# Performance work log

Hardware: AMD Instinct MI355X
Metric: run time of the kernel (lower is better)

Reference implementation:

```python
import jax, jax.numpy as jnp
import numpy as np

NUM_EDGES = 800_000
NUM_VERTICES = 100_000
NNZ = 1_600_000
D_MODEL = 128


def setup_inputs() -> dict:
    key = jax.random.key(0)
    ks = jax.random.split(key, 10)
    d = D_MODEL
    return {
        "x_e": jax.random.normal(ks[0], (NUM_EDGES, d), dtype=jnp.float32),
        "h_v": jax.random.normal(ks[1], (NUM_VERTICES, d), dtype=jnp.float32),
        "c_v": jax.random.normal(ks[2], (NUM_VERTICES, d), dtype=jnp.float32),
        "W_ih": jax.random.normal(ks[3], (4 * d, d), dtype=jnp.float32) * 0.05,
        "W_hh": jax.random.normal(ks[4], (4 * d, d), dtype=jnp.float32) * 0.05,
        "b_ih": jax.random.normal(ks[5], (4 * d,), dtype=jnp.float32) * 0.05,
        "b_hh": jax.random.normal(ks[6], (4 * d,), dtype=jnp.float32) * 0.05,
        "nnz_edge_ids": jax.random.randint(ks[7], (NNZ,), 0, NUM_EDGES, dtype=jnp.int32),
        "nnz_vertex_ids": jax.random.randint(ks[8], (NNZ,), 0, NUM_VERTICES, dtype=jnp.int32),
        "v_batch": jax.random.randint(ks[9], (NUM_VERTICES,), 0, 8, dtype=jnp.int32),
    }


def reference(x_e, h_v, c_v, W_ih, W_hh, b_ih, b_hh, nnz_edge_ids, nnz_vertex_ids, v_batch):
    # msg = adj_t.T @ x_e : scatter-add edge embeddings into incident vertices
    msg = jax.ops.segment_sum(x_e[nnz_edge_ids], nnz_vertex_ids,
                              num_segments=h_v.shape[0])  # [V, d]
    # single-step LSTM update (PyTorch gate order: i, f, g, o)
    gates = msg @ W_ih.T + b_ih + h_v @ W_hh.T + b_hh  # [V, 4d]
    i, f, g, o = jnp.split(gates, 4, axis=-1)
    i = jax.nn.sigmoid(i)
    f = jax.nn.sigmoid(f)
    g = jnp.tanh(g)
    o = jax.nn.sigmoid(o)
    c_new = f * c_v + i * g
    h_new = o * jnp.tanh(c_new)
    return (h_new, c_new)
```

## Files before the change

### kernel.cpp

```cpp
#include <hip/hip_runtime.h>
#include <hip/hip_bf16.h>

#define NE 800000
#define NV 100000
#define NNZN 1600000
#define D 128
#define SLOT_CAP 64

typedef short short8 __attribute__((ext_vector_type(8)));
typedef short s16x4 __attribute__((ext_vector_type(4)));
typedef float f32x4 __attribute__((ext_vector_type(4)));
typedef int   i32x4 __attribute__((ext_vector_type(4)));

__device__ __forceinline__ unsigned short f2bfu(float f) {
  union { float f; unsigned u; } x;
  x.f = f;
  unsigned u = x.u;
  u += ((u >> 16) & 1u) + 0x7FFFu;
  return (unsigned short)(u >> 16);
}

__device__ __forceinline__ float fsigmoid(float x) {
  return 1.0f / (1.0f + __expf(-x));
}
__device__ __forceinline__ float ftanh(float x) {
  return 2.0f / (1.0f + __expf(-2.0f * x)) - 1.0f;
}

__global__ __launch_bounds__(256) void wconv_kernel(
    const float* __restrict__ W_ih, const float* __restrict__ W_hh,
    const float* __restrict__ b_ih, const float* __restrict__ b_hh,
    short* __restrict__ Wcat, float* __restrict__ bcomb,
    int* __restrict__ counts) {
  int idx = blockIdx.x * 256 + threadIdx.x;
  if (idx < 16384) {
    int c8 = idx;
    int pos = c8 & 63;
    int t   = (c8 >> 6) & 1;
    int g   = (c8 >> 7) & 3;
    int kk  = (c8 >> 9) & 7;
    int wid = (c8 >> 12) & 3;
    int n = g * 128 + wid * 32 + t * 16 + (pos >> 2);
    int k0 = kk * 32 + (pos & 3) * 8;
    const float* src = (k0 < 128) ? (W_ih + (size_t)n * 128 + k0)
                                  : (W_hh + (size_t)n * 128 + (k0 - 128));
    f32x4 a = *(const f32x4*)(src);
    f32x4 b = *(const f32x4*)(src + 4);
    short8 v;
    v[0] = (short)f2bfu(a[0]); v[1] = (short)f2bfu(a[1]);
    v[2] = (short)f2bfu(a[2]); v[3] = (short)f2bfu(a[3]);
    v[4] = (short)f2bfu(b[0]); v[5] = (short)f2bfu(b[1]);
    v[6] = (short)f2bfu(b[2]); v[7] = (short)f2bfu(b[3]);
    *(short8*)(Wcat + (size_t)c8 * 8) = v;
  }
  if (idx < 512) bcomb[idx] = b_ih[idx] + b_hh[idx];
  if (idx < NV) counts[idx] = 0;
}

__global__ __launch_bounds__(256) void scatter_direct_kernel(
    const int* __restrict__ eid, const int* __restrict__ vid,
    int* __restrict__ counts, int* __restrict__ slots) {
  int j = blockIdx.x * 256 + threadIdx.x;
  if (j < NNZN) {
    int v = vid[j];
    int pos = atomicAdd(&counts[v], 1);
    if (pos < SLOT_CAP) slots[(size_t)v * SLOT_CAP + pos] = eid[j];
  }
}

__global__ __launch_bounds__(256, 6) void gather_kernel(
    const float* __restrict__ x_e, const int* __restrict__ counts,
    const int* __restrict__ slots, char* __restrict__ msgb) {
  __shared__ int slds[4][SLOT_CAP];
  const int tid = threadIdx.x;
  const int wid = tid >> 6;
  const int lane = tid & 63;
  const int v = blockIdx.x * 4 + wid;
  const int half = lane >> 5;
  const int pos = lane & 31;
  int deg = counts[v];
  deg = deg > SLOT_CAP ? SLOT_CAP : deg;
  slds[wid][lane] = slots[(size_t)v * SLOT_CAP + lane];
  const int* row_ids = slds[wid];

  f32x4 a0 = {0.f, 0.f, 0.f, 0.f}, a1 = a0, a2 = a0, a3 = a0;
  const int nfull = deg >> 4;
  const int rem = deg & 15;
#pragma unroll 1
  for (int c = 0; c < nfull; ++c) {
    int b = c * 16 + half;
    int e0 = row_ids[b];      int e1 = row_ids[b + 2];
    int e2 = row_ids[b + 4];  int e3 = row_ids[b + 6];
    int e4 = row_ids[b + 8];  int e5 = row_ids[b + 10];
    int e6 = row_ids[b + 12]; int e7 = row_ids[b + 14];
    f32x4 t0 = *(const f32x4*)(x_e + (size_t)e0 * D + pos * 4);
    f32x4 t1 = *(const f32x4*)(x_e + (size_t)e1 * D + pos * 4);
    f32x4 t2 = *(const f32x4*)(x_e + (size_t)e2 * D + pos * 4);
    f32x4 t3 = *(const f32x4*)(x_e + (size_t)e3 * D + pos * 4);
    f32x4 t4 = *(const f32x4*)(x_e + (size_t)e4 * D + pos * 4);
    f32x4 t5 = *(const f32x4*)(x_e + (size_t)e5 * D + pos * 4);
    f32x4 t6 = *(const f32x4*)(x_e + (size_t)e6 * D + pos * 4);
    f32x4 t7 = *(const f32x4*)(x_e + (size_t)e7 * D + pos * 4);
    a0 += t0; a1 += t1; a2 += t2; a3 += t3;
    a0 += t4; a1 += t5; a2 += t6; a3 += t7;
  }
  if (rem) {
    int b = nfull * 16 + half;
    f32x4 z = {0.f, 0.f, 0.f, 0.f};
    int i0 = b,      i1 = b + 2,  i2 = b + 4,  i3 = b + 6;
    int i4 = b + 8,  i5 = b + 10, i6 = b + 12, i7 = b + 14;
    int e0 = row_ids[i0 < deg ? i0 : 0];
    int e1 = row_ids[i1 < deg ? i1 : 0];
    int e2 = row_ids[i2 < deg ? i2 : 0];
    int e3 = row_ids[i3 < deg ? i3 : 0];
    int e4 = row_ids[i4 < deg ? i4 : 0];
    int e5 = row_ids[i5 < deg ? i5 : 0];
    int e6 = row_ids[i6 < deg ? i6 : 0];
    int e7 = row_ids[i7 < deg ? i7 : 0];
    f32x4 t0 = *(const f32x4*)(x_e + (size_t)e0 * D + pos * 4);
    f32x4 t1 = *(const f32x4*)(x_e + (size_t)e1 * D + pos * 4);
    f32x4 t2 = *(const f32x4*)(x_e + (size_t)e2 * D + pos * 4);
    f32x4 t3 = *(const f32x4*)(x_e + (size_t)e3 * D + pos * 4);
    f32x4 t4 = *(const f32x4*)(x_e + (size_t)e4 * D + pos * 4);
    f32x4 t5 = *(const f32x4*)(x_e + (size_t)e5 * D + pos * 4);
    f32x4 t6 = *(const f32x4*)(x_e + (size_t)e6 * D + pos * 4);
    f32x4 t7 = *(const f32x4*)(x_e + (size_t)e7 * D + pos * 4);
    a0 += (i0 < deg) ? t0 : z;
    a1 += (i1 < deg) ? t1 : z;
    a2 += (i2 < deg) ? t2 : z;
    a3 += (i3 < deg) ? t3 : z;
    a0 += (i4 < deg) ? t4 : z;
    a1 += (i5 < deg) ? t5 : z;
    a2 += (i6 < deg) ? t6 : z;
    a3 += (i7 < deg) ? t7 : z;
  }
  a0 += a1;
  a2 += a3;
  a0 += a2;
  f32x4 b;
  b[0] = __shfl_xor(a0[0], 32);
  b[1] = __shfl_xor(a0[1], 32);
  b[2] = __shfl_xor(a0[2], 32);
  b[3] = __shfl_xor(a0[3], 32);
  a0 += b;
  if (half == 0) {
    s16x4 p;
    p[0] = (short)f2bfu(a0[0]);
    p[1] = (short)f2bfu(a0[1]);
    p[2] = (short)f2bfu(a0[2]);
    p[3] = (short)f2bfu(a0[3]);
    *(s16x4*)(msgb + (size_t)v * 512 + pos * 8) = p;
  }
}

__global__ __launch_bounds__(256) void lstm_kernel(
    const char* __restrict__ msgb, const float* __restrict__ h_v,
    const float* __restrict__ c_v, const short* __restrict__ Wcat,
    const float* __restrict__ bcomb, float* __restrict__ out) {
  __shared__ char Atile[32 * 256 * 2];
  const int tid = threadIdx.x;
  const int vbase = blockIdx.x * 32;

#pragma unroll
  for (int i = 0; i < 4; ++i) {
    int cid = tid + i * 256;
    int row = cid >> 5;
    int c = cid & 31;
    short8 v;
    if (c < 16) {
      v = *(const short8*)(msgb + (size_t)(vbase + row) * 512 + c * 16);
    } else {
      const float* src = h_v + (size_t)(vbase + row) * D + (c - 16) * 8;
      f32x4 a = *(const f32x4*)(src);
      f32x4 b = *(const f32x4*)(src + 4);
      v[0] = (short)f2bfu(a[0]); v[1] = (short)f2bfu(a[1]);
      v[2] = (short)f2bfu(a[2]); v[3] = (short)f2bfu(a[3]);
      v[4] = (short)f2bfu(b[0]); v[5] = (short)f2bfu(b[1]);
      v[6] = (short)f2bfu(b[2]); v[7] = (short)f2bfu(b[3]);
    }
    int byteoff = (row * 512 + c * 16) ^ ((row & 7) << 4);
    *(short8*)(Atile + byteoff) = v;
  }
  __syncthreads();

  const int wid = tid >> 6;
  const int lane = tid & 63;
  const int l16 = lane & 15;
  const int lhi = lane >> 4;

  f32x4 acc[2][4][2] = {};

#pragma unroll
  for (int kk = 0; kk < 8; ++kk) {
    short8 afrag[2];
#pragma unroll
    for (int m = 0; m < 2; ++m) {
      int row = m * 16 + l16;
      int byteoff = (row * 512 + kk * 64 + lhi * 16) ^ ((row & 7) << 4);
      afrag[m] = *(const short8*)(Atile + byteoff);
    }
#pragma unroll
    for (int g = 0; g < 4; ++g) {
#pragma unroll
      for (int t = 0; t < 2; ++t) {
        size_t boff = (size_t)(wid * 64 + kk * 8 + g * 2 + t) * 1024
                    + (size_t)(l16 * 4 + lhi) * 16;
        short8 bfrag = *(const short8*)((const char*)Wcat + boff);
        acc[0][g][t] = __builtin_amdgcn_mfma_f32_16x16x32_bf16(afrag[0], bfrag, acc[0][g][t], 0, 0, 0);
        acc[1][g][t] = __builtin_amdgcn_mfma_f32_16x16x32_bf16(afrag[1], bfrag, acc[1][g][t], 0, 0, 0);
      }
    }
  }

  float* out_h = out;
  float* out_c = out + (size_t)NV * D;
#pragma unroll
  for (int m = 0; m < 2; ++m) {
#pragma unroll
    for (int t = 0; t < 2; ++t) {
      int d = wid * 32 + t * 16 + l16;
      float bi = bcomb[d];
      float bf = bcomb[128 + d];
      float bg = bcomb[256 + d];
      float bo = bcomb[384 + d];
#pragma unroll
      for (int r = 0; r < 4; ++r) {
        int v = vbase + m * 16 + lhi * 4 + r;
        float gi = acc[m][0][t][r] + bi;
        float gf = acc[m][1][t][r] + bf;
        float gg = acc[m][2][t][r] + bg;
        float go = acc[m][3][t][r] + bo;
        float ii = fsigmoid(gi);
        float ff = fsigmoid(gf);
        float g_ = ftanh(gg);
        float oo = fsigmoid(go);
        float cv = c_v[(size_t)v * D + d];
        float cn = ff * cv + ii * g_;
        float hn = oo * ftanh(cn);
        out_h[(size_t)v * D + d] = hn;
        out_c[(size_t)v * D + d] = cn;
      }
    }
  }
}

extern "C" void kernel_launch(void* const* d_in, const int* in_sizes, int n_in,
                              void* d_out, int out_size, void* d_ws, size_t ws_size,
                              hipStream_t stream) {
  const float* x_e  = (const float*)d_in[0];
  const float* h_v  = (const float*)d_in[1];
  const float* c_v  = (const float*)d_in[2];
  const float* W_ih = (const float*)d_in[3];
  const float* W_hh = (const float*)d_in[4];
  const float* b_ih = (const float*)d_in[5];
  const float* b_hh = (const float*)d_in[6];
  const int* eid    = (const int*)d_in[7];
  const int* vid    = (const int*)d_in[8];
  float* out = (float*)d_out;

  char* w = (char*)d_ws;
  short* Wcat  = (short*)w;                 w += 512 * 256 * sizeof(short);
  float* bcomb = (float*)w;                 w += 512 * sizeof(float);
  int* counts  = (int*)w;                   w += NV * sizeof(int);
  int* slots   = (int*)w;

  char* msgb = (char*)(out + (size_t)NV * D);

  wconv_kernel<<<512, 256, 0, stream>>>(W_ih, W_hh, b_ih, b_hh, Wcat, bcomb, counts);
  scatter_direct_kernel<<<(NNZN + 255) / 256, 256, 0, stream>>>(eid, vid, counts, slots);
  gather_kernel<<<NV / 4, 256, 0, stream>>>(x_e, counts, slots, msgb);
  lstm_kernel<<<NV / 32, 256, 0, stream>>>(msgb, h_v, c_v, Wcat, bcomb, out);
}
```

Before: 418.6 us.

## Split gather into two edge-range passes for cache locality

The gather runs as two passes, each touching only half of the x_e edge rows, so each pass works on about 205 MB of x_e instead of 410 MB and is meant to get better last-level cache hit rates. The first pass writes fp32 partial sums into the output buffer, and the second pass adds its half, converts to bf16 and writes msgb. The cost is reading counts and slots twice, extra partial-sum traffic, and wasted loads of a placeholder row for edges outside the range. Half the x_e set is still larger than MI355X's documented 256 MB Infinity Cache, so the locality gain may be small.

```diff
diff --git a/kernel.cpp b/kernel.cpp
--- a/kernel.cpp
+++ b/kernel.cpp
@@ -68,9 +68,11 @@
   }
 }
 
-__global__ __launch_bounds__(256, 6) void gather_kernel(
+template <bool FIRST>
+__global__ __launch_bounds__(256, 6) void gather_pass_kernel(
     const float* __restrict__ x_e, const int* __restrict__ counts,
-    const int* __restrict__ slots, char* __restrict__ msgb) {
+    const int* __restrict__ slots, float* __restrict__ pf,
+    char* __restrict__ msgb, int lo, int hi) {
   __shared__ int slds[4][SLOT_CAP];
   const int tid = threadIdx.x;
   const int wid = tid >> 6;
@@ -82,31 +84,14 @@
   deg = deg > SLOT_CAP ? SLOT_CAP : deg;
   slds[wid][lane] = slots[(size_t)v * SLOT_CAP + lane];
   const int* row_ids = slds[wid];
+  const float* clamp_row = x_e + (size_t)lo * D + pos * 4;
 
   f32x4 a0 = {0.f, 0.f, 0.f, 0.f}, a1 = a0, a2 = a0, a3 = a0;
-  const int nfull = deg >> 4;
-  const int rem = deg & 15;
+  const f32x4 z = a0;
+  const int nvol = (deg + 15) >> 4;
 #pragma unroll 1
-  for (int c = 0; c < nfull; ++c) {
+  for (int c = 0; c < nvol; ++c) {
     int b = c * 16 + half;
-    int e0 = row_ids[b];      int e1 = row_ids[b + 2];
-    int e2 = row_ids[b + 4];  int e3 = row_ids[b + 6];
-    int e4 = row_ids[b + 8];  int e5 = row_ids[b + 10];
-    int e6 = row_ids[b + 12]; int e7 = row_ids[b + 14];
-    f32x4 t0 = *(const f32x4*)(x_e + (size_t)e0 * D + pos * 4);
-    f32x4 t1 = *(const f32x4*)(x_e + (size_t)e1 * D + pos * 4);
-    f32x4 t2 = *(const f32x4*)(x_e + (size_t)e2 * D + pos * 4);
-    f32x4 t3 = *(const f32x4*)(x_e + (size_t)e3 * D + pos * 4);
-    f32x4 t4 = *(const f32x4*)(x_e + (size_t)e4 * D + pos * 4);
-    f32x4 t5 = *(const f32x4*)(x_e + (size_t)e5 * D + pos * 4);
-    f32x4 t6 = *(const f32x4*)(x_e + (size_t)e6 * D + pos * 4);
-    f32x4 t7 = *(const f32x4*)(x_e + (size_t)e7 * D + pos * 4);
-    a0 += t0; a1 += t1; a2 += t2; a3 += t3;
-    a0 += t4; a1 += t5; a2 += t6; a3 += t7;
-  }
-  if (rem) {
-    int b = nfull * 16 + half;
-    f32x4 z = {0.f, 0.f, 0.f, 0.f};
     int i0 = b,      i1 = b + 2,  i2 = b + 4,  i3 = b + 6;
     int i4 = b + 8,  i5 = b + 10, i6 = b + 12, i7 = b + 14;
     int e0 = row_ids[i0 < deg ? i0 : 0];
@@ -117,22 +102,30 @@
     int e5 = row_ids[i5 < deg ? i5 : 0];
     int e6 = row_ids[i6 < deg ? i6 : 0];
     int e7 = row_ids[i7 < deg ? i7 : 0];
-    f32x4 t0 = *(const f32x4*)(x_e + (size_t)e0 * D + pos * 4);
-    f32x4 t1 = *(const f32x4*)(x_e + (size_t)e1 * D + pos * 4);
-    f32x4 t2 = *(const f32x4*)(x_e + (size_t)e2 * D + pos * 4);
-    f32x4 t3 = *(const f32x4*)(x_e + (size_t)e3 * D + pos * 4);
-    f32x4 t4 = *(const f32x4*)(x_e + (size_t)e4 * D + pos * 4);
-    f32x4 t5 = *(const f32x4*)(x_e + (size_t)e5 * D + pos * 4);
-    f32x4 t6 = *(const f32x4*)(x_e + (size_t)e6 * D + pos * 4);
-    f32x4 t7 = *(const f32x4*)(x_e + (size_t)e7 * D + pos * 4);
-    a0 += (i0 < deg) ? t0 : z;
-    a1 += (i1 < deg) ? t1 : z;
-    a2 += (i2 < deg) ? t2 : z;
-    a3 += (i3 < deg) ? t3 : z;
-    a0 += (i4 < deg) ? t4 : z;
-    a1 += (i5 < deg) ? t5 : z;
-    a2 += (i6 < deg) ? t6 : z;
-    a3 += (i7 < deg) ? t7 : z;
+    bool v0 = (i0 < deg) && (e0 >= lo) && (e0 < hi);
+    bool v1 = (i1 < deg) && (e1 >= lo) && (e1 < hi);
+    bool v2 = (i2 < deg) && (e2 >= lo) && (e2 < hi);
+    bool v3 = (i3 < deg) && (e3 >= lo) && (e3 < hi);
+    bool v4 = (i4 < deg) && (e4 >= lo) && (e4 < hi);
+    bool v5 = (i5 < deg) && (e5 >= lo) && (e5 < hi);
+    bool v6 = (i6 < deg) && (e6 >= lo) && (e6 < hi);
+    bool v7 = (i7 < deg) && (e7 >= lo) && (e7 < hi);
+    f32x4 t0 = *(const f32x4*)(v0 ? x_e + (size_t)e0 * D + pos * 4 : clamp_row);
+    f32x4 t1 = *(const f32x4*)(v1 ? x_e + (size_t)e1 * D + pos * 4 : clamp_row);
+    f32x4 t2 = *(const f32x4*)(v2 ? x_e + (size_t)e2 * D + pos * 4 : clamp_row);
+    f32x4 t3 = *(const f32x4*)(v3 ? x_e + (size_t)e3 * D + pos * 4 : clamp_row);
+    f32x4 t4 = *(const f32x4*)(v4 ? x_e + (size_t)e4 * D + pos * 4 : clamp_row);
+    f32x4 t5 = *(const f32x4*)(v5 ? x_e + (size_t)e5 * D + pos * 4 : clamp_row);
+    f32x4 t6 = *(const f32x4*)(v6 ? x_e + (size_t)e6 * D + pos * 4 : clamp_row);
+    f32x4 t7 = *(const f32x4*)(v7 ? x_e + (size_t)e7 * D + pos * 4 : clamp_row);
+    a0 += v0 ? t0 : z;
+    a1 += v1 ? t1 : z;
+    a2 += v2 ? t2 : z;
+    a3 += v3 ? t3 : z;
+    a0 += v4 ? t4 : z;
+    a1 += v5 ? t5 : z;
+    a2 += v6 ? t6 : z;
+    a3 += v7 ? t7 : z;
   }
   a0 += a1;
   a2 += a3;
@@ -144,12 +137,18 @@
   b[3] = __shfl_xor(a0[3], 32);
   a0 += b;
   if (half == 0) {
-    s16x4 p;
-    p[0] = (short)f2bfu(a0[0]);
-    p[1] = (short)f2bfu(a0[1]);
-    p[2] = (short)f2bfu(a0[2]);
-    p[3] = (short)f2bfu(a0[3]);
-    *(s16x4*)(msgb + (size_t)v * 512 + pos * 8) = p;
+    if (FIRST) {
+      *(f32x4*)(pf + (size_t)v * D + pos * 4) = a0;
+    } else {
+      f32x4 p = *(const f32x4*)(pf + (size_t)v * D + pos * 4);
+      a0 += p;
+      s16x4 pk;
+      pk[0] = (short)f2bfu(a0[0]);
+      pk[1] = (short)f2bfu(a0[1]);
+      pk[2] = (short)f2bfu(a0[2]);
+      pk[3] = (short)f2bfu(a0[3]);
+      *(s16x4*)(msgb + (size_t)v * 512 + pos * 8) = pk;
+    }
   }
 }
 
@@ -264,10 +263,12 @@
   int* counts  = (int*)w;                   w += NV * sizeof(int);
   int* slots   = (int*)w;
 
+  float* pf = out;
   char* msgb = (char*)(out + (size_t)NV * D);
 
   wconv_kernel<<<512, 256, 0, stream>>>(W_ih, W_hh, b_ih, b_hh, Wcat, bcomb, counts);
   scatter_direct_kernel<<<(NNZN + 255) / 256, 256, 0, stream>>>(eid, vid, counts, slots);
-  gather_kernel<<<NV / 4, 256, 0, stream>>>(x_e, counts, slots, msgb);
+  gather_pass_kernel<true><<<NV / 4, 256, 0, stream>>>(x_e, counts, slots, pf, msgb, 0, NE / 2);
+  gather_pass_kernel<false><<<NV / 4, 256, 0, stream>>>(x_e, counts, slots, pf, msgb, NE / 2, NE);
   lstm_kernel<<<NV / 32, 256, 0, stream>>>(msgb, h_v, c_v, Wcat, bcomb, out);
 }
```

New measurement: 445.8 us. +6.5%, slower.

## Convert x_e to fp16 during scatter and gather half-precision rows

Applied to the files above, without the earlier changes.

A new fused kernel builds the slot lists with atomics and also converts the full edge embedding table to fp16 in a grid-stride loop. The gather then reads 16-byte fp16 chunks, so each row load moves half the bytes, and it accumulates in fp32. The aim is to cut the random-access gather traffic, paid for by a full streaming read and write of x_e (about 400MB in, 200MB out) and some loss of input precision. The fp32 path stays as a fallback when the workspace is too small, and its occupancy hint changes from 6 to 4.

```diff
diff --git a/kernel.cpp b/kernel.cpp
--- a/kernel.cpp
+++ b/kernel.cpp
@@ -6,11 +6,13 @@
 #define NNZN 1600000
 #define D 128
 #define SLOT_CAP 64
+#define SC_BLOCKS 8192
 
 typedef short short8 __attribute__((ext_vector_type(8)));
 typedef short s16x4 __attribute__((ext_vector_type(4)));
 typedef float f32x4 __attribute__((ext_vector_type(4)));
-typedef int   i32x4 __attribute__((ext_vector_type(4)));
+typedef float f32x8 __attribute__((ext_vector_type(8)));
+typedef _Float16 h8v __attribute__((ext_vector_type(8)));
 
 __device__ __forceinline__ unsigned short f2bfu(float f) {
   union { float f; unsigned u; } x;
@@ -25,6 +27,13 @@
 }
 __device__ __forceinline__ float ftanh(float x) {
   return 2.0f / (1.0f + __expf(-2.0f * x)) - 1.0f;
+}
+
+__device__ __forceinline__ f32x8 h2f8(h8v h) {
+  f32x8 r;
+#pragma unroll
+  for (int k = 0; k < 8; ++k) r[k] = (float)h[k];
+  return r;
 }
 
 __global__ __launch_bounds__(256) void wconv_kernel(
@@ -57,6 +66,29 @@
   if (idx < NV) counts[idx] = 0;
 }
 
+__global__ __launch_bounds__(256) void scatcon_kernel(
+    const int* __restrict__ eid, const int* __restrict__ vid,
+    int* __restrict__ counts, int* __restrict__ slots,
+    const float* __restrict__ x_e, _Float16* __restrict__ x_h) {
+  unsigned j = blockIdx.x * 256 + threadIdx.x;
+  if (j < NNZN) {
+    int v = vid[j];
+    int pos = atomicAdd(&counts[v], 1);
+    if (pos < SLOT_CAP) slots[(size_t)v * SLOT_CAP + pos] = eid[j];
+  }
+  const unsigned NU = (unsigned)NE * 16u;
+  for (unsigned u = j; u < NU; u += SC_BLOCKS * 256u) {
+    f32x4 a = __builtin_nontemporal_load((const f32x4*)(x_e + (size_t)u * 8));
+    f32x4 b = __builtin_nontemporal_load((const f32x4*)(x_e + (size_t)u * 8 + 4));
+    h8v h;
+    h[0] = (_Float16)a[0]; h[1] = (_Float16)a[1];
+    h[2] = (_Float16)a[2]; h[3] = (_Float16)a[3];
+    h[4] = (_Float16)b[0]; h[5] = (_Float16)b[1];
+    h[6] = (_Float16)b[2]; h[7] = (_Float16)b[3];
+    *(h8v*)(x_h + (size_t)u * 8) = h;
+  }
+}
+
 __global__ __launch_bounds__(256) void scatter_direct_kernel(
     const int* __restrict__ eid, const int* __restrict__ vid,
     int* __restrict__ counts, int* __restrict__ slots) {
@@ -68,7 +100,92 @@
   }
 }
 
-__global__ __launch_bounds__(256, 6) void gather_kernel(
+__global__ __launch_bounds__(256, 4) void gather16_kernel(
+    const _Float16* __restrict__ x_h, const int* __restrict__ counts,
+    const int* __restrict__ slots, char* __restrict__ msgb) {
+  __shared__ int slds[4][SLOT_CAP];
+  const int tid = threadIdx.x;
+  const int wid = tid >> 6;
+  const int lane = tid & 63;
+  const int v = blockIdx.x * 4 + wid;
+  const int grp = lane >> 4;
+  const int p16 = lane & 15;
+  int deg = counts[v];
+  deg = deg > SLOT_CAP ? SLOT_CAP : deg;
+  slds[wid][lane] = slots[(size_t)v * SLOT_CAP + lane];
+  const int* row_ids = slds[wid];
+
+  f32x8 A0 = {0.f,0.f,0.f,0.f,0.f,0.f,0.f,0.f};
+  f32x8 A1 = A0, A2 = A0, A3 = A0;
+  const f32x8 Z = A0;
+  const int nfull = deg >> 5;
+  const int rem = deg & 31;
+#pragma unroll 1
+  for (int c = 0; c < nfull; ++c) {
+    int b = c * 32 + grp;
+    int e0 = row_ids[b];      int e1 = row_ids[b + 4];
+    int e2 = row_ids[b + 8];  int e3 = row_ids[b + 12];
+    int e4 = row_ids[b + 16]; int e5 = row_ids[b + 20];
+    int e6 = row_ids[b + 24]; int e7 = row_ids[b + 28];
+    h8v t0 = *(const h8v*)(x_h + (size_t)e0 * D + p16 * 8);
+    h8v t1 = *(const h8v*)(x_h + (size_t)e1 * D + p16 * 8);
+    h8v t2 = *(const h8v*)(x_h + (size_t)e2 * D + p16 * 8);
+    h8v t3 = *(const h8v*)(x_h + (size_t)e3 * D + p16 * 8);
+    h8v t4 = *(const h8v*)(x_h + (size_t)e4 * D + p16 * 8);
+    h8v t5 = *(const h8v*)(x_h + (size_t)e5 * D + p16 * 8);
+    h8v t6 = *(const h8v*)(x_h + (size_t)e6 * D + p16 * 8);
+    h8v t7 = *(const h8v*)(x_h + (size_t)e7 * D + p16 * 8);
+    A0 += h2f8(t0); A1 += h2f8(t1); A2 += h2f8(t2); A3 += h2f8(t3);
+    A0 += h2f8(t4); A1 += h2f8(t5); A2 += h2f8(t6); A3 += h2f8(t7);
+  }
+  if (rem) {
+    int b = nfull * 32 + grp;
+    int i0 = b,      i1 = b + 4,  i2 = b + 8,  i3 = b + 12;
+    int i4 = b + 16, i5 = b + 20, i6 = b + 24, i7 = b + 28;
+    int e0 = row_ids[i0 < deg ? i0 : 0];
+    int e1 = row_ids[i1 < deg ? i1 : 0];
+    int e2 = row_ids[i2 < deg ? i2 : 0];
+    int e3 = row_ids[i3 < deg ? i3 : 0];
+    int e4 = row_ids[i4 < deg ? i4 : 0];
+    int e5 = row_ids[i5 < deg ? i5 : 0];
+    int e6 = row_ids[i6 < deg ? i6 : 0];
+    int e7 = row_ids[i7 < deg ? i7 : 0];
+    h8v t0 = *(const h8v*)(x_h + (size_t)e0 * D + p16 * 8);
+    h8v t1 = *(const h8v*)(x_h + (size_t)e1 * D + p16 * 8);
+    h8v t2 = *(const h8v*)(x_h + (size_t)e2 * D + p16 * 8);
+    h8v t3 = *(const h8v*)(x_h + (size_t)e3 * D + p16 * 8);
+    h8v t4 = *(const h8v*)(x_h + (size_t)e4 * D + p16 * 8);
+    h8v t5 = *(const h8v*)(x_h + (size_t)e5 * D + p16 * 8);
+    h8v t6 = *(const h8v*)(x_h + (size_t)e6 * D + p16 * 8);
+    h8v t7 = *(const h8v*)(x_h + (size_t)e7 * D + p16 * 8);
+    A0 += (i0 < deg) ? h2f8(t0) : Z;
+    A1 += (i1 < deg) ? h2f8(t1) : Z;
+    A2 += (i2 < deg) ? h2f8(t2) : Z;
+    A3 += (i3 < deg) ? h2f8(t3) : Z;
+    A0 += (i4 < deg) ? h2f8(t4) : Z;
+    A1 += (i5 < deg) ? h2f8(t5) : Z;
+    A2 += (i6 < deg) ? h2f8(t6) : Z;
+    A3 += (i7 < deg) ? h2f8(t7) : Z;
+  }
+  A0 += A1;
+  A2 += A3;
+  A0 += A2;
+#pragma unroll
+  for (int f = 0; f < 8; ++f) {
+    float x = A0[f];
+    x += __shfl_xor(x, 32);
+    x += __shfl_xor(x, 16);
+    A0[f] = x;
+  }
+  if (lane < 16) {
+    short8 p;
+#pragma unroll
+    for (int f = 0; f < 8; ++f) p[f] = (short)f2bfu(A0[f]);
+    *(short8*)(msgb + (size_t)v * 512 + p16 * 16) = p;
+  }
+}
+
+__global__ __launch_bounds__(256, 4) void gather_kernel(
     const float* __restrict__ x_e, const int* __restrict__ counts,
     const int* __restrict__ slots, char* __restrict__ msgb) {
   __shared__ int slds[4][SLOT_CAP];
@@ -93,16 +210,14 @@
     int e2 = row_ids[b + 4];  int e3 = row_ids[b + 6];
     int e4 = row_ids[b + 8];  int e5 = row_ids[b + 10];
     int e6 = row_ids[b + 12]; int e7 = row_ids[b + 14];
-    f32x4 t0 = *(const f32x4*)(x_e + (size_t)e0 * D + pos * 4);
-    f32x4 t1 = *(const f32x4*)(x_e + (size_t)e1 * D + pos * 4);
-    f32x4 t2 = *(const f32x4*)(x_e + (size_t)e2 * D + pos * 4);
-    f32x4 t3 = *(const f32x4*)(x_e + (size_t)e3 * D + pos * 4);
-    f32x4 t4 = *(const f32x4*)(x_e + (size_t)e4 * D + pos * 4);
-    f32x4 t5 = *(const f32x4*)(x_e + (size_t)e5 * D + pos * 4);
-    f32x4 t6 = *(const f32x4*)(x_e + (size_t)e6 * D + pos * 4);
-    f32x4 t7 = *(const f32x4*)(x_e + (size_t)e7 * D + pos * 4);
-    a0 += t0; a1 += t1; a2 += t2; a3 += t3;
-    a0 += t4; a1 += t5; a2 += t6; a3 += t7;
+    a0 += *(const f32x4*)(x_e + (size_t)e0 * D + pos * 4);
+    a1 += *(const f32x4*)(x_e + (size_t)e1 * D + pos * 4);
+    a2 += *(const f32x4*)(x_e + (size_t)e2 * D + pos * 4);
+    a3 += *(const f32x4*)(x_e + (size_t)e3 * D + pos * 4);
+    a0 += *(const f32x4*)(x_e + (size_t)e4 * D + pos * 4);
+    a1 += *(const f32x4*)(x_e + (size_t)e5 * D + pos * 4);
+    a2 += *(const f32x4*)(x_e + (size_t)e6 * D + pos * 4);
+    a3 += *(const f32x4*)(x_e + (size_t)e7 * D + pos * 4);
   }
   if (rem) {
     int b = nfull * 16 + half;
@@ -262,12 +377,23 @@
   short* Wcat  = (short*)w;                 w += 512 * 256 * sizeof(short);
   float* bcomb = (float*)w;                 w += 512 * sizeof(float);
   int* counts  = (int*)w;                   w += NV * sizeof(int);
-  int* slots   = (int*)w;
+  int* slots   = (int*)w;                   w += (size_t)NV * SLOT_CAP * sizeof(int);
+  _Float16* x_h = (_Float16*)w;
+
+  const size_t need = 512 * 256 * sizeof(short) + 512 * sizeof(float)
+                    + (size_t)NV * sizeof(int)
+                    + (size_t)NV * SLOT_CAP * sizeof(int)
+                    + (size_t)NE * D * sizeof(_Float16);
 
   char* msgb = (char*)(out + (size_t)NV * D);
 
   wconv_kernel<<<512, 256, 0, stream>>>(W_ih, W_hh, b_ih, b_hh, Wcat, bcomb, counts);
-  scatter_direct_kernel<<<(NNZN + 255) / 256, 256, 0, stream>>>(eid, vid, counts, slots);
-  gather_kernel<<<NV / 4, 256, 0, stream>>>(x_e, counts, slots, msgb);
+  if (ws_size >= need) {
+    scatcon_kernel<<<SC_BLOCKS, 256, 0, stream>>>(eid, vid, counts, slots, x_e, x_h);
+    gather16_kernel<<<NV / 4, 256, 0, stream>>>(x_h, counts, slots, msgb);
+  } else {
+    scatter_direct_kernel<<<(NNZN + 255) / 256, 256, 0, stream>>>(eid, vid, counts, slots);
+    gather_kernel<<<NV / 4, 256, 0, stream>>>(x_e, counts, slots, msgb);
+  }
   lstm_kernel<<<NV / 32, 256, 0, stream>>>(msgb, h_v, c_v, Wcat, bcomb, out);
 }
```

Measured after the change: 419.1 us. About the same (+0.1%).
